# Kernel optimization log

Hardware: AMD Instinct MI355X
Metric: run time of the kernel (lower is better)

The kernel has to match this reference:

```python
import jax, jax.numpy as jnp
import numpy as np

MEAN = 0.1307
SIGMA = 0.3081
BINARY_ITER = 10
SIG_SCALE = 5.0


def spu(x):
    # SPU(x) = x^2 - 0.5 for x >= 0, sigmoid(-x) - 1 for x < 0 (continuous at 0)
    return jnp.where(x >= 0, x * x - 0.5, jax.nn.sigmoid(-x) - 1.0)


def joining_line(x1, y1, x2, y2):
    slope = (y2 - y1) / (x2 - x1)
    return slope, y2 - slope * x2


def parabola_tangent(x):
    return 2.0 * x, -x * x - 0.5


def parabola_tangent_through(x1, y1):
    D = 4.0 * x1 * x1 - 4.0 * y1 - 2.0
    x2 = (2.0 * x1 + jnp.sqrt(jnp.clip(D, 0.0))) / 2.0
    return parabola_tangent(x2)


def sigmoid_tangent(x):
    s = jax.nn.sigmoid(x)
    slope = -s * (1.0 - s)
    return slope, -s - slope * x


def binary_search_point(lx, ux, uy):
    L = lx
    R = jnp.zeros_like(lx)
    for _ in range(BINARY_ITER):  # fixed 10-iteration search, unrolled
        m = 0.5 * (L + R)
        sm, im = sigmoid_tangent(m)
        mask = sm * ux + im - uy > 0
        L = jnp.where(mask, m, L)
        R = jnp.where(mask, R, m)
    return L


def line_to_constraint(slope, intercept):
    # [n, n+1]: diagonal slope matrix with intercept as last column (matches torch diagflat/cat)
    return jnp.concatenate([jnp.diagflat(slope), intercept[:, None]], axis=1)


def analyze_affine(W, b, ub, lb):
    constr = jnp.concatenate([W, b[:, None]], axis=1)
    bu = jnp.where(W > 0, ub[None, :], lb[None, :])
    bl = jnp.where(W > 0, lb[None, :], ub[None, :])
    return constr, jnp.einsum('ij,ij->i', bu, W) + b, jnp.einsum('ij,ij->i', bl, W) + b


def analyze_spu(ux, lx):
    uy = spu(ux)
    ly = spu(lx)
    new_ub = jnp.maximum(uy, ly)
    sj, ij = joining_line(lx, ly, ux, uy)
    right = lx > 0
    left = ux <= 0
    crossing = (~left) & (~right)
    # learned positions at their (fresh) init: sigmoid(0) -> midpoint
    mid = 0.5 * (ux + lx)
    sp, ip = parabola_tangent(mid)
    ssm, ism = sigmoid_tangent(mid)
    new_lb = jnp.where(crossing, jnp.full_like(uy, -0.5), jnp.minimum(uy, ly))
    # crossing-case lower constraint
    spu_, ipu = parabola_tangent(ux)
    limit = spu_ * lx + ipu
    clm = (jnp.abs(lx) > ux).astype(lx.dtype)
    clp = jax.nn.sigmoid((clm - 0.5) * 2.0 * SIG_SCALE) * (ly - limit) + limit
    ptm = clp < -0.5
    spt, ipt = parabola_tangent_through(lx, clp)
    sjn, ijn = joining_line(lx, clp, jnp.zeros_like(lx), jnp.full_like(lx, -0.5))
    s_cl = jnp.where(ptm, spt, sjn)
    i_cl = jnp.where(ptm, ipt, ijn)
    # crossing-case upper constraint
    ssl, isl = sigmoid_tangent(lx)
    stv = ssl * ux + isl - uy
    L = binary_search_point(lx, ux, uy)
    scp = jax.nn.sigmoid(-SIG_SCALE) * (L - lx) + lx
    ssc, isc = sigmoid_tangent(scp)
    up_mask = stv > 0
    s_cu = jnp.where(up_mask, ssc, sj)
    i_cu = jnp.where(up_mask, isc, ij)
    rf = right.astype(lx.dtype)
    lf = left.astype(lx.dtype)
    cf = crossing.astype(lx.dtype)
    us = rf * sj + lf * ssm + cf * s_cu
    ui = rf * ij + lf * ism + cf * i_cu
    ls = rf * sp + lf * sj + cf * s_cl
    li = rf * ip + lf * ij + cf * i_cl
    return line_to_constraint(us, ui), line_to_constraint(ls, li), new_ub, new_lb


def back_substitute(uc, lc, ub, lb):
    cu, cl = uc[-1], lc[-1]
    for pu, pl in zip(uc[-2::-1], lc[-2::-1]):
        # where(curr>0, prev_upper, prev_lower) contracted with curr == split pos/neg matmuls
        Wu, bu = cu[:, :-1], cu[:, -1]
        cu = jnp.maximum(Wu, 0.0) @ pu + jnp.minimum(Wu, 0.0) @ pl
        cu = cu.at[:, -1].add(bu)
        Wl, bl = cl[:, :-1], cl[:, -1]
        cl = jnp.maximum(Wl, 0.0) @ pl + jnp.minimum(Wl, 0.0) @ pu
        cl = cl.at[:, -1].add(bl)
    return jnp.minimum(ub, cu[:, 0]), jnp.maximum(lb, cl[:, 0])


def setup_inputs() -> dict:
    key = jax.random.key(0)
    ks = jax.random.split(key, 9)
    d_in, h, d_out = 784, 2048, 10
    inputs = jax.random.uniform(ks[0], (d_in,), dtype=jnp.float32)
    eps = jnp.float32(0.05)
    w1 = jax.random.normal(ks[1], (h, d_in), dtype=jnp.float32) / np.sqrt(d_in).astype(np.float32)
    b1 = jax.random.normal(ks[2], (h,), dtype=jnp.float32) * 0.1
    w2 = jax.random.normal(ks[3], (h, h), dtype=jnp.float32) / np.sqrt(h).astype(np.float32)
    b2 = jax.random.normal(ks[4], (h,), dtype=jnp.float32) * 0.1
    w3 = jax.random.normal(ks[5], (h, h), dtype=jnp.float32) / np.sqrt(h).astype(np.float32)
    b3 = jax.random.normal(ks[6], (h,), dtype=jnp.float32) * 0.1
    w4 = jax.random.normal(ks[7], (d_out, h), dtype=jnp.float32) / np.sqrt(h).astype(np.float32)
    b4 = jax.random.normal(ks[8], (d_out,), dtype=jnp.float32) * 0.1
    return {"inputs": inputs, "eps": eps, "w1": w1, "b1": b1, "w2": w2, "b2": b2,
            "w3": w3, "b3": b3, "w4": w4, "b4": b4}


def reference(inputs, eps, w1, b1, w2, b2, w3, b3, w4, b4):
    ub = [jnp.clip(inputs + eps, None, 1.0)]
    lb = [jnp.clip(inputs - eps, 0.0)]
    # normalization layer: applied in place to bounds and input constraint ([784,1])
    uc = [((ub[0] - MEAN) / SIGMA)[:, None]]
    lc = [((lb[0] - MEAN) / SIGMA)[:, None]]
    ub[0] = (ub[0] - MEAN) / SIGMA
    lb[0] = (lb[0] - MEAN) / SIGMA
    weights = [(w1, b1), (w2, b2), (w3, b3), (w4, b4)]
    for i, (W, b) in enumerate(weights):
        c, u, l = analyze_affine(W, b, ub[-1], lb[-1])
        uc.append(c)
        lc.append(c)
        ub.append(u)
        lb.append(l)
        u, l = back_substitute(uc, lc, ub[-1], lb[-1])
        ub[-1], lb[-1] = u, l
        if i < len(weights) - 1:
            cu_, cl_, u, l = analyze_spu(ub[-1], lb[-1])
            uc.append(cu_)
            lc.append(cl_)
            ub.append(u)
            lb.append(l)
            u, l = back_substitute(uc, lc, ub[-1], lb[-1])
            ub[-1], lb[-1] = u, l
    return lb[-1].min()
```

## Files before the change

kernel.cpp:

```cpp
#include <hip/hip_runtime.h>
#include <cstdint>
#include <cstddef>

#define MEAN_C 0.1307f
#define SIGMA_C 0.3081f
#define SIG_SCALE_C 5.0f

typedef __bf16 bf16_t;
typedef __bf16 bf16x8 __attribute__((ext_vector_type(8)));
typedef __bf16 bf16x4 __attribute__((ext_vector_type(4)));
typedef float f32x4 __attribute__((ext_vector_type(4)));

__device__ __forceinline__ f32x4 mfma16(bf16x8 a, bf16x8 b, f32x4 c) {
    return __builtin_amdgcn_mfma_f32_16x16x32_bf16(a, b, c, 0, 0, 0);
}

typedef const __attribute__((address_space(1))) void* gvp;
typedef __attribute__((address_space(3))) void* lvp;
__device__ __forceinline__ void g2l16(const void* g, void* l) {
    __builtin_amdgcn_global_load_lds((gvp)g, (lvp)l, 16, 0, 0);
}

__device__ __forceinline__ size_t swz(int r, int k, int ktiles) {
    return (((size_t)(r >> 4) * ktiles + (k >> 5)) << 9)
         + (((k >> 3) & 3) << 7) + ((r & 15) << 3) + (k & 7);
}

#define KTILES 64


__device__ __forceinline__ float sigmoidf_(float x) {
    if (x >= 0.f) { float e = __expf(-x); return 1.f / (1.f + e); }
    float e = __expf(x); return e / (1.f + e);
}

__device__ __forceinline__ float spu_f(float x) {
    return (x >= 0.f) ? (x * x - 0.5f) : (sigmoidf_(-x) - 1.f);
}

__device__ __forceinline__ float wave_sum(float a) {
    #pragma unroll
    for (int o = 32; o > 0; o >>= 1) a += __shfl_xor(a, o, 64);
    return a;
}

__device__ __forceinline__ void spu_body(int i, int n,
        float iUi, float iLi, float vU, float vL,
        float* __restrict__ us, float* __restrict__ ui,
        float* __restrict__ ls, float* __restrict__ li,
        float* __restrict__ pU, float* __restrict__ pL) {
    float ux = fminf(iUi, vU);
    float lx = fmaxf(iLi, vL);
    float uy = spu_f(ux), ly = spu_f(lx);
    float new_ub = fmaxf(uy, ly);
    float sj = (uy - ly) / (ux - lx);
    float ij = uy - sj * ux;
    bool right = lx > 0.f;
    bool left = ux <= 0.f;
    float mid = 0.5f * (ux + lx);
    float sp = 2.f * mid, ip = -mid * mid - 0.5f;
    float sm = sigmoidf_(mid);
    float ssm = -sm * (1.f - sm);
    float ism = -sm - ssm * mid;
    bool crossing = (!left) && (!right);
    float new_lb = crossing ? -0.5f : fminf(uy, ly);
    float spu_s = 2.f * ux, ipu = -ux * ux - 0.5f;
    float limit = spu_s * lx + ipu;
    float clm = (fabsf(lx) > ux) ? 1.f : 0.f;
    float clp = sigmoidf_((clm - 0.5f) * 2.f * SIG_SCALE_C) * (ly - limit) + limit;
    bool ptm = clp < -0.5f;
    float D = 4.f * lx * lx - 4.f * clp - 2.f;
    float x2 = (2.f * lx + sqrtf(fmaxf(D, 0.f))) * 0.5f;
    float spt = 2.f * x2, ipt = -x2 * x2 - 0.5f;
    float sjn = (clp + 0.5f) / lx;
    float ijn = -0.5f;
    float s_cl = ptm ? spt : sjn;
    float i_cl = ptm ? ipt : ijn;
    float sl = sigmoidf_(lx);
    float ssl = -sl * (1.f - sl);
    float isl = -sl - ssl * lx;
    float stv = ssl * ux + isl - uy;
    float Lb = lx, Rb = 0.f;
    #pragma unroll
    for (int t = 0; t < 10; ++t) {
        float mm = 0.5f * (Lb + Rb);
        float smm = sigmoidf_(mm);
        float sms = -smm * (1.f - smm);
        float smi = -smm - sms * mm;
        bool mask = (sms * ux + smi - uy) > 0.f;
        Lb = mask ? mm : Lb;
        Rb = mask ? Rb : mm;
    }
    float scp = sigmoidf_(-SIG_SCALE_C) * (Lb - lx) + lx;
    float sc = sigmoidf_(scp);
    float ssc = -sc * (1.f - sc);
    float isc = -sc - ssc * scp;
    bool up = stv > 0.f;
    float s_cu = up ? ssc : sj;
    float i_cu = up ? isc : ij;
    float usv, uiv, lsv, liv;
    if (right)      { usv = sj;   uiv = ij;   lsv = sp;   liv = ip;   }
    else if (left)  { usv = ssm;  uiv = ism;  lsv = sj;   liv = ij;   }
    else            { usv = s_cu; uiv = i_cu; lsv = s_cl; liv = i_cl; }
    us[i] = usv; ui[i] = uiv; ls[i] = lsv; li[i] = liv;
    float vu = (usv >= 0.f) ? vU : vL;
    float vl = (lsv >= 0.f) ? vL : vU;
    pU[i] = fminf(new_ub, usv * vu + uiv);
    pL[i] = fmaxf(new_lb, lsv * vl + liv);
}


__global__ __launch_bounds__(256) void k_interval_affine(
        const float* __restrict__ W, const float* __restrict__ b,
        const float* __restrict__ U, const float* __restrict__ L,
        int m, int nrows, float* __restrict__ uo, float* __restrict__ lo) {
    int r = (blockIdx.x << 2) + (threadIdx.x >> 6);
    if (r >= nrows) return;
    int lane = threadIdx.x & 63;
    const f32x4* Wr = (const f32x4*)(W + (size_t)r * m);
    const f32x4* U4 = (const f32x4*)U;
    const f32x4* L4 = (const f32x4*)L;
    int nf4 = m >> 2;
    float au = 0.f, al = 0.f;
    for (int j = lane; j < nf4; j += 64) {
        f32x4 wv = Wr[j], uu = U4[j], ll = L4[j];
        #pragma unroll
        for (int u = 0; u < 4; ++u) {
            float w = wv[u];
            float hi = (w > 0.f) ? uu[u] : ll[u];
            float lo2 = (w > 0.f) ? ll[u] : uu[u];
            au = fmaf(w, hi, au);
            al = fmaf(w, lo2, al);
        }
    }
    au = wave_sum(au); al = wave_sum(al);
    if (lane == 0) { uo[r] = au + b[r]; lo[r] = al + b[r]; }
}

__global__ void k_spu2(const float* __restrict__ iU, const float* __restrict__ iL,
                       const float* __restrict__ vraw, int n,
                       float* __restrict__ us, float* __restrict__ ui,
                       float* __restrict__ ls, float* __restrict__ li,
                       float* __restrict__ pU, float* __restrict__ pL) {
    int i = blockIdx.x * blockDim.x + threadIdx.x;
    if (i >= n) return;
    spu_body(i, n, iU[i], iL[i], vraw[i], vraw[n + i], us, ui, ls, li, pU, pL);
}


__global__ __launch_bounds__(256) void k_wT3(
        const float* __restrict__ W1, const float* __restrict__ W2,
        const float* __restrict__ W3,
        bf16_t* __restrict__ W1t, bf16_t* __restrict__ W2t, bf16_t* __restrict__ W3t,
        const float* __restrict__ x, const float* __restrict__ eps,
        float* __restrict__ ubn, float* __restrict__ lbn) {
    __shared__ bf16_t t[64 * 65];
    int z = blockIdx.z;
    const float* W; int N, ldw; bf16_t* Wt;
    if (z == 0)      { W = W2; N = 2048; ldw = 2048; Wt = W2t; }
    else if (z == 1) { W = W3; N = 2048; ldw = 2048; Wt = W3t; }
    else {
        W = W1; N = 784; ldw = 784; Wt = W1t;
        if (blockIdx.y >= 14) {
            if (blockIdx.y == 14 && blockIdx.x == 0) {
                for (int i = threadIdx.x; i < 896; i += 256) {
                    if (i >= 784) { ubn[i] = 0.f; lbn[i] = 0.f; }
                    else {
                        float e = eps[0];
                        float ub = fminf(x[i] + e, 1.f);
                        float lb = fmaxf(x[i] - e, 0.f);
                        ubn[i] = (ub - MEAN_C) / SIGMA_C;
                        lbn[i] = (lb - MEAN_C) / SIGMA_C;
                    }
                }
            }
            return;
        }
    }
    int k0 = blockIdx.x * 64, n0 = blockIdx.y * 64;
    int tid = threadIdx.x;
    int rg = tid >> 4;
    int cg = (tid & 15) * 4;
    bool fast = (n0 + 64 <= N);
    #pragma unroll
    for (int it = 0; it < 4; ++it) {
        int row = it * 16 + rg;
        const float* Wr = W + (size_t)(k0 + row) * ldw + n0 + cg;
        float v0, v1, v2, v3;
        if (fast) {
            f32x4 vv = *(const f32x4*)Wr;
            v0 = vv[0]; v1 = vv[1]; v2 = vv[2]; v3 = vv[3];
        } else {
            v0 = (n0 + cg + 0 < N) ? Wr[0] : 0.f;
            v1 = (n0 + cg + 1 < N) ? Wr[1] : 0.f;
            v2 = (n0 + cg + 2 < N) ? Wr[2] : 0.f;
            v3 = (n0 + cg + 3 < N) ? Wr[3] : 0.f;
        }
        t[(cg + 0) * 65 + row] = (bf16_t)v0;
        t[(cg + 1) * 65 + row] = (bf16_t)v1;
        t[(cg + 2) * 65 + row] = (bf16_t)v2;
        t[(cg + 3) * 65 + row] = (bf16_t)v3;
    }
    __syncthreads();
    #pragma unroll
    for (int p = 0; p < 2; ++p) {
        int c = tid + p * 256;
        int lr = c & 63, lq = c >> 6;
        bf16x8 v;
        #pragma unroll
        for (int u = 0; u < 8; ++u) v[u] = t[lr * 65 + lq * 8 + u];
        *(bf16x8*)(Wt + swz(n0 + lr, k0 + lq * 8, KTILES)) = v;
    }
}

__global__ __launch_bounds__(256) void k_prep16(
        const float* __restrict__ W, const float* __restrict__ b, int n,
        const float* __restrict__ cus, const float* __restrict__ cui,
        const float* __restrict__ cls, const float* __restrict__ cli,
        const float* __restrict__ bvec,
        const float* __restrict__ U, const float* __restrict__ L,
        bf16_t* __restrict__ Ab, float* __restrict__ av,
        float* __restrict__ iU, float* __restrict__ iL) {
    int rt = blockIdx.x;
    int tid = threadIdx.x, lane = tid & 63, wid = tid >> 6;
    int mrow = lane & 15, q = lane >> 4;
    int r = rt * 16 + mrow;
    bool act = r < 2 * n;
    bool isU = r < n;
    int i = act ? (isU ? r : r - n) : 0;
    float gate = act ? 1.f : 0.f;
    const float* Wr = W + (size_t)i * 2048;
    const float* ps = isU ? cus : cls;
    const float* ns = isU ? cls : cus;
    const float* yi = isU ? cui : cli;
    const float* zi = isU ? cli : cui;
    const float* hi = isU ? U : L;
    const float* lo = isU ? L : U;
    float a = 0.f, a2 = 0.f;
    bf16_t* Abase = Ab + ((size_t)rt * KTILES) * 512 + lane * 8;
    for (int kt = wid; kt < KTILES; kt += 4) {
        int k0 = kt * 32 + q * 8;
        bf16x8 ov;
        #pragma unroll
        for (int h = 0; h < 2; ++h) {
            int kb = k0 + 4 * h;
            f32x4 wv = *(const f32x4*)(Wr + kb);
            f32x4 p0 = *(const f32x4*)(ps + kb);
            f32x4 q0 = *(const f32x4*)(ns + kb);
            f32x4 y0 = *(const f32x4*)(yi + kb);
            f32x4 z0 = *(const f32x4*)(zi + kb);
            f32x4 c0 = *(const f32x4*)(bvec + kb);
            f32x4 h0 = *(const f32x4*)(hi + kb);
            f32x4 l0 = *(const f32x4*)(lo + kb);
            #pragma unroll
            for (int u = 0; u < 4; ++u) {
                float w = gate * wv[u];
                float pos = fmaxf(w, 0.f), neg = fminf(w, 0.f);
                float mx = pos * p0[u] + neg * q0[u];
                ov[4 * h + u] = (bf16_t)mx;
                a += pos * y0[u] + neg * z0[u] + mx * c0[u];
                a2 += pos * h0[u] + neg * l0[u];
            }
        }
        *(bf16x8*)(Abase + (size_t)kt * 512) = ov;
    }
    a += __shfl_xor(a, 16, 64);  a += __shfl_xor(a, 32, 64);
    a2 += __shfl_xor(a2, 16, 64); a2 += __shfl_xor(a2, 32, 64);
    __shared__ float sh[2][4][16];
    if (lane < 16) { sh[0][wid][lane] = a; sh[1][wid][lane] = a2; }
    __syncthreads();
    if (tid < 16) {
        int r2 = rt * 16 + tid;
        float ta = sh[0][0][tid] + sh[0][1][tid] + sh[0][2][tid] + sh[0][3][tid];
        float tb = sh[1][0][tid] + sh[1][1][tid] + sh[1][2][tid] + sh[1][3][tid];
        if (r2 < 2 * n) {
            bool isU2 = r2 < n;
            int i2 = isU2 ? r2 : r2 - n;
            av[r2] = ta + b[i2];
            if (isU2) iU[i2] = tb + b[i2];
            else      iL[i2] = tb + b[i2];
        } else {
            av[r2] = 0.f;
        }
    }
}

__global__ __launch_bounds__(256) void k_colmix16(
        const bf16_t* __restrict__ Cb, int ldc, int splits, size_t sstride, int n,
        int tpb,
        const float* __restrict__ cus, const float* __restrict__ cui,
        const float* __restrict__ cls, const float* __restrict__ cli,
        const float* __restrict__ bvec,
        bf16_t* __restrict__ Ab, float* __restrict__ av) {
    int rt = blockIdx.x;
    int kt0 = blockIdx.y * tpb;
    int tid = threadIdx.x, lane = tid & 63, wid = tid >> 6;
    int mrow = lane & 15, q = lane >> 4;
    int r = rt * 16 + mrow;
    bool isU = r < n;
    const bf16_t* Cr = Cb + (size_t)r * ldc;
    const float* ps = isU ? cus : cls;
    const float* ns = isU ? cls : cus;
    const float* yi = isU ? cui : cli;
    const float* zi = isU ? cli : cui;
    float a = 0.f;
    bf16_t* Abase = Ab + ((size_t)rt * KTILES) * 512 + lane * 8;
    for (int kt = kt0 + wid; kt < kt0 + tpb; kt += 4) {
        int k0 = kt * 32 + q * 8;
        float wsum[8] = {0.f, 0.f, 0.f, 0.f, 0.f, 0.f, 0.f, 0.f};
        for (int s = 0; s < splits; ++s) {
            bf16x8 v = *(const bf16x8*)(Cr + s * sstride + k0);
            #pragma unroll
            for (int u = 0; u < 8; ++u) wsum[u] += (float)v[u];
        }
        f32x4 p0 = *(const f32x4*)(ps + k0), p1 = *(const f32x4*)(ps + k0 + 4);
        f32x4 q0 = *(const f32x4*)(ns + k0), q1 = *(const f32x4*)(ns + k0 + 4);
        f32x4 y0 = *(const f32x4*)(yi + k0), y1 = *(const f32x4*)(yi + k0 + 4);
        f32x4 z0 = *(const f32x4*)(zi + k0), z1 = *(const f32x4*)(zi + k0 + 4);
        f32x4 c0 = *(const f32x4*)(bvec + k0), c1 = *(const f32x4*)(bvec + k0 + 4);
        bf16x8 ov;
        #pragma unroll
        for (int u = 0; u < 4; ++u) {
            float w = wsum[u];
            float pos = fmaxf(w, 0.f), neg = fminf(w, 0.f);
            float mx = pos * p0[u] + neg * q0[u];
            ov[u] = (bf16_t)mx;
            a += pos * y0[u] + neg * z0[u] + mx * c0[u];
        }
        #pragma unroll
        for (int u = 0; u < 4; ++u) {
            float w = wsum[4 + u];
            float pos = fmaxf(w, 0.f), neg = fminf(w, 0.f);
            float mx = pos * p1[u] + neg * q1[u];
            ov[4 + u] = (bf16_t)mx;
            a += pos * y1[u] + neg * z1[u] + mx * c1[u];
        }
        *(bf16x8*)(Abase + (size_t)kt * 512) = ov;
    }
    a += __shfl_xor(a, 16, 64);
    a += __shfl_xor(a, 32, 64);
    __shared__ float sh[4][16];
    if (lane < 16) sh[wid][lane] = a;
    __syncthreads();
    if (tid < 16) {
        float tot = sh[0][tid] + sh[1][tid] + sh[2][tid] + sh[3][tid];
        atomicAdd(&av[rt * 16 + tid], tot);
    }
}

__global__ __launch_bounds__(640) void k_reduce16f(
        const bf16_t* __restrict__ Cb, int ldc, int m, int n,
        int splits, size_t sstride,
        const float* __restrict__ av,
        const float* __restrict__ ubn, const float* __restrict__ lbn,
        const float* __restrict__ iL,
        float* __restrict__ out) {
    __shared__ float sbl[16];
    int tid = threadIdx.x, lane = tid & 63, wv = tid >> 6;
    int nch = m >> 3;
    int i = wv;
    int r = n + i;
    const bf16_t* Cr = Cb + (size_t)r * ldc;
    const float* p = lbn;
    const float* q = ubn;
    float a = 0.f;
    for (int c = lane; c < nch; c += 64) {
        float wsum[8] = {0.f, 0.f, 0.f, 0.f, 0.f, 0.f, 0.f, 0.f};
        for (int s = 0; s < splits; ++s) {
            bf16x8 v = *(const bf16x8*)(Cr + s * sstride + c * 8);
            #pragma unroll
            for (int u = 0; u < 8; ++u) wsum[u] += (float)v[u];
        }
        f32x4 p0 = *(const f32x4*)(p + c * 8), p1 = *(const f32x4*)(p + c * 8 + 4);
        f32x4 q0 = *(const f32x4*)(q + c * 8), q1 = *(const f32x4*)(q + c * 8 + 4);
        #pragma unroll
        for (int u = 0; u < 4; ++u) {
            a += fmaxf(wsum[u], 0.f) * p0[u] + fminf(wsum[u], 0.f) * q0[u];
            a += fmaxf(wsum[4 + u], 0.f) * p1[u] + fminf(wsum[4 + u], 0.f) * q1[u];
        }
    }
    a = wave_sum(a);
    if (lane == 0) sbl[i] = fmaxf(iL[i], a + av[r]);
    __syncthreads();
    if (tid < 64) {
        float v = 3.4e38f;
        for (int j = lane; j < n; j += 64) v = fminf(v, sbl[j]);
        #pragma unroll
        for (int o = 32; o > 0; o >>= 1) v = fminf(v, __shfl_down(v, o, 64));
        if (lane == 0) out[0] = v;
    }
}


#define GEMM_PIPE()                                                            \
    int tid = threadIdx.x, lane = tid & 63, w = tid >> 6;                      \
    int wm = w & 1, wn = w >> 1;                                               \
    f32x4 acc[4][4];                                                           \
    _Pragma("unroll")                                                          \
    for (int i = 0; i < 4; ++i)                                                \
        _Pragma("unroll")                                                      \
        for (int j = 0; j < 4; ++j) acc[i][j] = (f32x4){0.f, 0.f, 0.f, 0.f};   \
    auto stage = [&](int kk) {                                                 \
        int b = kk & 1;                                                        \
        size_t go = (size_t)kk * 1024;                                         \
        bf16_t* la = &As2[b * 8192 + w * 1024];                                \
        bf16_t* lb = &Bs2[b * 8192 + w * 1024];                                \
        g2l16(a0 + go, la);          g2l16(a0 + go + 512, la + 512);           \
        g2l16(a1 + go, la + 4096);   g2l16(a1 + go + 512, la + 4608);          \
        g2l16(b0 + go, lb);          g2l16(b0 + go + 512, lb + 512);           \
        g2l16(b1 + go, lb + 4096);   g2l16(b1 + go + 512, lb + 4608);          \
    };                                                                         \
    stage(0); stage(1);                                                        \
    asm volatile("s_waitcnt vmcnt(8)" ::: "memory");                           \
    __builtin_amdgcn_s_barrier();                                              \
    for (int kk = 0; kk < nk; ++kk) {                                          \
        const bf16_t* cA = &As2[(kk & 1) * 8192];                              \
        const bf16_t* cB = &Bs2[(kk & 1) * 8192];                              \
        bf16x8 af0[4], af1[4], bq0[4], bq1[4];                                 \
        _Pragma("unroll")                                                      \
        for (int i = 0; i < 4; ++i) {                                          \
            af0[i] = *(const bf16x8*)(cA + (wm * 4 + i) * 1024 + lane * 8);    \
            af1[i] = *(const bf16x8*)(cA + (wm * 4 + i) * 1024 + 512 + lane * 8); \
            bq0[i] = *(const bf16x8*)(cB + (wn * 4 + i) * 1024 + lane * 8);    \
            bq1[i] = *(const bf16x8*)(cB + (wn * 4 + i) * 1024 + 512 + lane * 8); \
        }                                                                      \
        asm volatile("s_waitcnt lgkmcnt(0)" ::: "memory");                     \
        __builtin_amdgcn_s_barrier();                                          \
        if (kk + 2 < nk) stage(kk + 2);                                        \
        _Pragma("unroll")                                                      \
        for (int i = 0; i < 4; ++i)                                            \
            _Pragma("unroll")                                                  \
            for (int j = 0; j < 4; ++j)                                        \
                acc[i][j] = mfma16(bq0[j], af0[i], acc[i][j]);                 \
        _Pragma("unroll")                                                      \
        for (int i = 0; i < 4; ++i)                                            \
            _Pragma("unroll")                                                  \
            for (int j = 0; j < 4; ++j)                                        \
                acc[i][j] = mfma16(bq1[j], af1[i], acc[i][j]);                 \
        if (kk + 2 < nk) asm volatile("s_waitcnt vmcnt(8)" ::: "memory");      \
        else             asm volatile("s_waitcnt vmcnt(0)" ::: "memory");      \
        __builtin_amdgcn_s_barrier();                                          \
    }

__global__ __launch_bounds__(256) void k_gemm16(
        const bf16_t* __restrict__ A, const bf16_t* __restrict__ Bt,
        bf16_t* __restrict__ C, int ldc, size_t sstride, int nk) {
    __shared__ __align__(16) bf16_t As2[16384];
    __shared__ __align__(16) bf16_t Bs2[16384];
    int tr0 = blockIdx.y * 8, tc0 = blockIdx.x * 8;
    int kt0 = blockIdx.z * nk * 2;
    int wtmp = threadIdx.x >> 6, ltmp = threadIdx.x & 63;
    const bf16_t* a0 = A + (((size_t)(tr0 + wtmp)     * KTILES + kt0) << 9) + ltmp * 8;
    const bf16_t* a1 = A + (((size_t)(tr0 + wtmp + 4) * KTILES + kt0) << 9) + ltmp * 8;
    const bf16_t* b0 = Bt + (((size_t)(tc0 + wtmp)     * KTILES + kt0) << 9) + ltmp * 8;
    const bf16_t* b1 = Bt + (((size_t)(tc0 + wtmp + 4) * KTILES + kt0) << 9) + ltmp * 8;
    GEMM_PIPE()
    bf16_t* Cz = C + (size_t)blockIdx.z * sstride;
    int orow = lane & 15, ocol = (lane >> 4) * 4;
    size_t row0 = (size_t)blockIdx.y * 128;
    size_t col0 = (size_t)blockIdx.x * 128;
    #pragma unroll
    for (int i = 0; i < 4; ++i) {
        size_t gr = row0 + wm * 64 + i * 16 + orow;
        #pragma unroll
        for (int j = 0; j < 4; ++j) {
            size_t gc = col0 + wn * 64 + j * 16 + ocol;
            bf16x4 v;
            #pragma unroll
            for (int rg = 0; rg < 4; ++rg) v[rg] = (bf16_t)acc[i][j][rg];
            *(bf16x4*)(Cz + gr * (size_t)ldc + gc) = v;
        }
    }
}

__global__ __launch_bounds__(256) void k_gemm16_mix(
        const bf16_t* __restrict__ A, const bf16_t* __restrict__ Bt, int n,
        const float* __restrict__ cus, const float* __restrict__ cui,
        const float* __restrict__ cls, const float* __restrict__ cli,
        const float* __restrict__ bvec,
        bf16_t* __restrict__ Ab2, float* __restrict__ av, int nk) {
    __shared__ __align__(16) bf16_t As2[16384];
    __shared__ __align__(16) bf16_t Bs2[16384];
    __shared__ float asum[2][128];
    int wg = (int)(blockIdx.y * gridDim.x + blockIdx.x);
    int xcd = wg & 7, idx = wg >> 3;
    int bm = (xcd & 3) * 8 + (idx & 7);
    int bn = (xcd >> 2) * 8 + (idx >> 3);
    int tr0 = bm * 8, tc0 = bn * 8;
    int wtmp = threadIdx.x >> 6, ltmp = threadIdx.x & 63;
    const bf16_t* a0 = A + (((size_t)(tr0 + wtmp)     * KTILES) << 9) + ltmp * 8;
    const bf16_t* a1 = A + (((size_t)(tr0 + wtmp + 4) * KTILES) << 9) + ltmp * 8;
    const bf16_t* b0 = Bt + (((size_t)(tc0 + wtmp)     * KTILES) << 9) + ltmp * 8;
    const bf16_t* b1 = Bt + (((size_t)(tc0 + wtmp + 4) * KTILES) << 9) + ltmp * 8;
    GEMM_PIPE()
    size_t row0 = (size_t)bm * 128;
    size_t col0 = (size_t)bn * 128;
    bool isU = (int)row0 < n;
    const float* ps = isU ? cus : cls;
    const float* ns = isU ? cls : cus;
    const float* yi = isU ? cui : cli;
    const float* zi = isU ? cli : cui;
    int orow = lane & 15, ocol = (lane >> 4) * 4;
    #pragma unroll
    for (int i = 0; i < 4; ++i) {
        int gr = (int)row0 + wm * 64 + i * 16 + orow;
        float ra = 0.f;
        #pragma unroll
        for (int j = 0; j < 4; ++j) {
            int gc = (int)col0 + wn * 64 + j * 16 + ocol;
            f32x4 p0 = *(const f32x4*)(ps + gc);
            f32x4 q0 = *(const f32x4*)(ns + gc);
            f32x4 y0 = *(const f32x4*)(yi + gc);
            f32x4 z0 = *(const f32x4*)(zi + gc);
            f32x4 c0 = *(const f32x4*)(bvec + gc);
            bf16x4 ov;
            #pragma unroll
            for (int rg = 0; rg < 4; ++rg) {
                float v = acc[i][j][rg];
                float pos = fmaxf(v, 0.f), neg = fminf(v, 0.f);
                float mx = pos * p0[rg] + neg * q0[rg];
                ov[rg] = (bf16_t)mx;
                ra += pos * y0[rg] + neg * z0[rg] + mx * c0[rg];
            }
            *(bf16x4*)(Ab2 + swz(gr, gc, KTILES)) = ov;
        }
        ra += __shfl_xor(ra, 16, 64);
        ra += __shfl_xor(ra, 32, 64);
        if (lane < 16) asum[wn][wm * 64 + i * 16 + lane] = ra;
    }
    __syncthreads();
    if (tid < 128) atomicAdd(&av[row0 + tid], asum[0][tid] + asum[1][tid]);
}

__global__ __launch_bounds__(256) void k_gemm16_red(
        const bf16_t* __restrict__ A, const bf16_t* __restrict__ Bt, int n,
        const float* __restrict__ ubn, const float* __restrict__ lbn,
        float* __restrict__ av, int nk) {
    __shared__ __align__(16) bf16_t As2[16384];
    __shared__ __align__(16) bf16_t Bs2[16384];
    __shared__ float asum[2][128];
    int wg = (int)(blockIdx.y * gridDim.x + blockIdx.x);
    int id = (wg & 7) * 28 + (wg >> 3);
    int bm = id / 7, bn = id % 7;
    int tr0 = bm * 8, tc0 = bn * 8;
    int wtmp = threadIdx.x >> 6, ltmp = threadIdx.x & 63;
    const bf16_t* a0 = A + (((size_t)(tr0 + wtmp)     * KTILES) << 9) + ltmp * 8;
    const bf16_t* a1 = A + (((size_t)(tr0 + wtmp + 4) * KTILES) << 9) + ltmp * 8;
    const bf16_t* b0 = Bt + (((size_t)(tc0 + wtmp)     * KTILES) << 9) + ltmp * 8;
    const bf16_t* b1 = Bt + (((size_t)(tc0 + wtmp + 4) * KTILES) << 9) + ltmp * 8;
    GEMM_PIPE()
    size_t row0 = (size_t)bm * 128;
    size_t col0 = (size_t)bn * 128;
    bool isU = (int)row0 < n;
    const float* p = isU ? ubn : lbn;
    const float* q = isU ? lbn : ubn;
    int ocol = (lane >> 4) * 4;
    #pragma unroll
    for (int i = 0; i < 4; ++i) {
        float ra = 0.f;
        #pragma unroll
        for (int j = 0; j < 4; ++j) {
            int gc = (int)col0 + wn * 64 + j * 16 + ocol;
            f32x4 p0 = *(const f32x4*)(p + gc);
            f32x4 q0 = *(const f32x4*)(q + gc);
            #pragma unroll
            for (int rg = 0; rg < 4; ++rg) {
                float v = acc[i][j][rg];
                ra += fmaxf(v, 0.f) * p0[rg] + fminf(v, 0.f) * q0[rg];
            }
        }
        ra += __shfl_xor(ra, 16, 64);
        ra += __shfl_xor(ra, 32, 64);
        if (lane < 16) asum[wn][wm * 64 + i * 16 + lane] = ra;
    }
    __syncthreads();
    if (tid < 128) atomicAdd(&av[row0 + tid], asum[0][tid] + asum[1][tid]);
}


extern "C" void kernel_launch(void* const* d_in, const int* in_sizes, int n_in,
                              void* d_out, int out_size, void* d_ws, size_t ws_size,
                              hipStream_t stream) {
    (void)in_sizes; (void)n_in; (void)out_size; (void)ws_size;
    const float* x   = (const float*)d_in[0];
    const float* eps = (const float*)d_in[1];
    const float* W1  = (const float*)d_in[2];
    const float* B1  = (const float*)d_in[3];
    const float* W2  = (const float*)d_in[4];
    const float* B2  = (const float*)d_in[5];
    const float* W3  = (const float*)d_in[6];
    const float* B3  = (const float*)d_in[7];
    const float* W4  = (const float*)d_in[8];
    const float* B4  = (const float*)d_in[9];
    float* out = (float*)d_out;

    const int H = 2048, DIN = 784, DOUT = 10;
    const int NP1 = 896;
    const int MP4 = 128;

    float* ws = (float*)d_ws;
    size_t off = 0;
    auto alloc = [&](size_t nf) -> float* {
        float* p = ws + off;
        off += (nf + 3) & ~(size_t)3;
        return p;
    };
    float* ubn = alloc(NP1);
    float* lbn = alloc(NP1);
    float* vraw1 = alloc(2 * H);
    float* us1 = alloc(H); float* ui1 = alloc(H); float* ls1 = alloc(H); float* li1 = alloc(H);
    float* pU1 = alloc(H); float* pL1 = alloc(H);
    float* iU2 = alloc(H); float* iL2 = alloc(H);
    float* us2 = alloc(H); float* ui2 = alloc(H); float* ls2 = alloc(H); float* li2 = alloc(H);
    float* pU2 = alloc(H); float* pL2 = alloc(H);
    float* iU3 = alloc(H); float* iL3 = alloc(H);
    float* us3 = alloc(H); float* ui3 = alloc(H); float* ls3 = alloc(H); float* li3 = alloc(H);
    float* pU3 = alloc(H); float* pL3 = alloc(H);
    float* iU4 = alloc(32); float* iL4 = alloc(32);
    float* av  = alloc(2 * H);
    bf16_t* Ab  = (bf16_t*)alloc((size_t)2 * H * H / 2);
    bf16_t* Ab2 = (bf16_t*)alloc((size_t)2 * H * H / 2);
    bf16_t* W1t = (bf16_t*)alloc((size_t)NP1 * H / 2);
    bf16_t* W2t = (bf16_t*)alloc((size_t)H * H / 2);
    bf16_t* W3t = (bf16_t*)alloc((size_t)H * H / 2);
    bf16_t* Cs  = (bf16_t*)alloc((size_t)16 * MP4 * H / 2);

    dim3 blk(256);

    k_wT3<<<dim3(32, 32, 3), blk, 0, stream>>>(W1, W2, W3, W1t, W2t, W3t,
                                               x, eps, ubn, lbn);

    size_t ss4H = (size_t)MP4 * H;
    size_t ss4N = (size_t)MP4 * NP1;

    k_interval_affine<<<dim3(H / 4), blk, 0, stream>>>(W1, B1, ubn, lbn, DIN, H,
                                                       vraw1, vraw1 + H);
    k_spu2<<<dim3(H / 64), dim3(64), 0, stream>>>(vraw1, vraw1 + H, vraw1, H,
        us1, ui1, ls1, li1, pU1, pL1);

    k_prep16<<<dim3(2 * H / 16), blk, 0, stream>>>(W2, B2, H,
        us1, ui1, ls1, li1, B1, pU1, pL1, Ab, av, iU2, iL2);
    k_gemm16_red<<<dim3(2 * H / 128, NP1 / 128), blk, 0, stream>>>(Ab, W1t, H,
        ubn, lbn, av, KTILES / 2);
    k_spu2<<<dim3(H / 64), dim3(64), 0, stream>>>(iU2, iL2, av, H,
        us2, ui2, ls2, li2, pU2, pL2);

    k_prep16<<<dim3(2 * H / 16), blk, 0, stream>>>(W3, B3, H,
        us2, ui2, ls2, li2, B2, pU2, pL2, Ab, av, iU3, iL3);
    k_gemm16_mix<<<dim3(2 * H / 128, H / 128), blk, 0, stream>>>(Ab, W2t, H,
        us1, ui1, ls1, li1, B1, Ab2, av, KTILES / 2);
    k_gemm16_red<<<dim3(2 * H / 128, NP1 / 128), blk, 0, stream>>>(Ab2, W1t, H,
        ubn, lbn, av, KTILES / 2);
    k_spu2<<<dim3(H / 64), dim3(64), 0, stream>>>(iU3, iL3, av, H,
        us3, ui3, ls3, li3, pU3, pL3);

    k_prep16<<<dim3(MP4 / 16), blk, 0, stream>>>(W4, B4, DOUT,
        us3, ui3, ls3, li3, B3, pU3, pL3, Ab, av, iU4, iL4);
    k_gemm16<<<dim3(H / 128, MP4 / 128, 16), blk, 0, stream>>>(Ab, W3t, Cs, H, ss4H, 2);
    k_colmix16<<<dim3(MP4 / 16, 8), blk, 0, stream>>>(Cs, H, 16, ss4H, DOUT, KTILES / 8,
        us2, ui2, ls2, li2, B2, Ab2, av);
    k_gemm16<<<dim3(H / 128, MP4 / 128, 16), blk, 0, stream>>>(Ab2, W2t, Cs, H, ss4H, 2);
    k_colmix16<<<dim3(MP4 / 16, 8), blk, 0, stream>>>(Cs, H, 16, ss4H, DOUT, KTILES / 8,
        us1, ui1, ls1, li1, B1, Ab, av);
    k_gemm16<<<dim3(NP1 / 128, MP4 / 128, 16), blk, 0, stream>>>(Ab, W1t, Cs, NP1, ss4N, 2);
    k_reduce16f<<<dim3(1), dim3(640), 0, stream>>>(Cs, NP1, DIN, DOUT, 16, ss4N,
        av, ubn, lbn, iL4, out);
}
```

Before: 329.5 us.

## Use 8-wave blocks in fused GEMMs and fuse first affine with SPU

The fused back-substitution GEMMs (mix and red) now launch 512 threads (8 waves) per 128x128 tile instead of 4. Each wave owns a 64x32 sub-tile and loads half as many LDS stages, which lowers per-wave accumulator registers and adds latency hiding. The epilogue reductions are widened to four column groups to match. Separately, the first interval-affine kernel now applies the SPU relaxation directly, removing one launch and an intermediate buffer.

```diff
diff --git a/kernel.cpp b/kernel.cpp
--- a/kernel.cpp
+++ b/kernel.cpp
@@ -110,12 +110,15 @@
 }
 
 
-__global__ __launch_bounds__(256) void k_interval_affine(
+__global__ __launch_bounds__(256) void k_interval_spu(
         const float* __restrict__ W, const float* __restrict__ b,
         const float* __restrict__ U, const float* __restrict__ L,
-        int m, int nrows, float* __restrict__ uo, float* __restrict__ lo) {
+        int m, int n,
+        float* __restrict__ us, float* __restrict__ ui,
+        float* __restrict__ ls, float* __restrict__ li,
+        float* __restrict__ pU, float* __restrict__ pL) {
     int r = (blockIdx.x << 2) + (threadIdx.x >> 6);
-    if (r >= nrows) return;
+    if (r >= n) return;
     int lane = threadIdx.x & 63;
     const f32x4* Wr = (const f32x4*)(W + (size_t)r * m);
     const f32x4* U4 = (const f32x4*)U;
@@ -134,7 +137,10 @@
         }
     }
     au = wave_sum(au); al = wave_sum(al);
-    if (lane == 0) { uo[r] = au + b[r]; lo[r] = al + b[r]; }
+    if (lane == 0) {
+        float vU = au + b[r], vL = al + b[r];
+        spu_body(r, n, vU, vL, vU, vL, us, ui, ls, li, pU, pL);
+    }
 }
 
 __global__ void k_spu2(const float* __restrict__ iU, const float* __restrict__ iL,
@@ -391,7 +397,6 @@
     }
 }
 
-
 #define GEMM_PIPE()                                                            \
     int tid = threadIdx.x, lane = tid & 63, w = tid >> 6;                      \
     int wm = w & 1, wn = w >> 1;                                               \
@@ -473,7 +478,58 @@
     }
 }
 
-__global__ __launch_bounds__(256) void k_gemm16_mix(
+#define GEMM_PIPE8()                                                           \
+    int tid = threadIdx.x, lane = tid & 63, w = tid >> 6;            \
+    int wm = w >> 2, wn = w & 3;                                               \
+    f32x4 acc[4][2];                                                           \
+    _Pragma("unroll")                                                          \
+    for (int i = 0; i < 4; ++i)                                                \
+        _Pragma("unroll")                                                      \
+        for (int j = 0; j < 2; ++j) acc[i][j] = (f32x4){0.f, 0.f, 0.f, 0.f};   \
+    auto stage = [&](int kk) {                                                 \
+        int b = kk & 1;                                                        \
+        size_t go = (size_t)kk * 1024;                                         \
+        bf16_t* la = &As2[b * 8192 + w * 1024];                                \
+        bf16_t* lb = &Bs2[b * 8192 + w * 1024];                                \
+        g2l16(a0 + go, la);   g2l16(a0 + go + 512, la + 512);                  \
+        g2l16(b0 + go, lb);   g2l16(b0 + go + 512, lb + 512);                  \
+    };                                                                         \
+    stage(0); stage(1);                                                        \
+    asm volatile("s_waitcnt vmcnt(4)" ::: "memory");                           \
+    __builtin_amdgcn_s_barrier();                                              \
+    for (int kk = 0; kk < nk; ++kk) {                                          \
+        const bf16_t* cA = &As2[(kk & 1) * 8192];                              \
+        const bf16_t* cB = &Bs2[(kk & 1) * 8192];                              \
+        bf16x8 af0[4], af1[4], bq0[2], bq1[2];                                 \
+        _Pragma("unroll")                                                      \
+        for (int i = 0; i < 4; ++i) {                                          \
+            af0[i] = *(const bf16x8*)(cA + (wm * 4 + i) * 1024 + lane * 8);    \
+            af1[i] = *(const bf16x8*)(cA + (wm * 4 + i) * 1024 + 512 + lane * 8); \
+        }                                                                      \
+        _Pragma("unroll")                                                      \
+        for (int j = 0; j < 2; ++j) {                                          \
+            bq0[j] = *(const bf16x8*)(cB + (wn * 2 + j) * 1024 + lane * 8);    \
+            bq1[j] = *(const bf16x8*)(cB + (wn * 2 + j) * 1024 + 512 + lane * 8); \
+        }                                                                      \
+        asm volatile("s_waitcnt lgkmcnt(0)" ::: "memory");                     \
+        __builtin_amdgcn_s_barrier();                                          \
+        if (kk + 2 < nk) stage(kk + 2);                                        \
+        _Pragma("unroll")                                                      \
+        for (int i = 0; i < 4; ++i)                                            \
+            _Pragma("unroll")                                                  \
+            for (int j = 0; j < 2; ++j)                                        \
+                acc[i][j] = mfma16(bq0[j], af0[i], acc[i][j]);                 \
+        _Pragma("unroll")                                                      \
+        for (int i = 0; i < 4; ++i)                                            \
+            _Pragma("unroll")                                                  \
+            for (int j = 0; j < 2; ++j)                                        \
+                acc[i][j] = mfma16(bq1[j], af1[i], acc[i][j]);                 \
+        if (kk + 2 < nk) asm volatile("s_waitcnt vmcnt(4)" ::: "memory");      \
+        else             asm volatile("s_waitcnt vmcnt(0)" ::: "memory");      \
+        __builtin_amdgcn_s_barrier();                                          \
+    }
+
+__global__ __launch_bounds__(512, 4) void k_gemm16_mix(
         const bf16_t* __restrict__ A, const bf16_t* __restrict__ Bt, int n,
         const float* __restrict__ cus, const float* __restrict__ cui,
         const float* __restrict__ cls, const float* __restrict__ cli,
@@ -481,18 +537,16 @@
         bf16_t* __restrict__ Ab2, float* __restrict__ av, int nk) {
     __shared__ __align__(16) bf16_t As2[16384];
     __shared__ __align__(16) bf16_t Bs2[16384];
-    __shared__ float asum[2][128];
+    __shared__ float asum[4][128];
     int wg = (int)(blockIdx.y * gridDim.x + blockIdx.x);
     int xcd = wg & 7, idx = wg >> 3;
     int bm = (xcd & 3) * 8 + (idx & 7);
     int bn = (xcd >> 2) * 8 + (idx >> 3);
     int tr0 = bm * 8, tc0 = bn * 8;
     int wtmp = threadIdx.x >> 6, ltmp = threadIdx.x & 63;
-    const bf16_t* a0 = A + (((size_t)(tr0 + wtmp)     * KTILES) << 9) + ltmp * 8;
-    const bf16_t* a1 = A + (((size_t)(tr0 + wtmp + 4) * KTILES) << 9) + ltmp * 8;
-    const bf16_t* b0 = Bt + (((size_t)(tc0 + wtmp)     * KTILES) << 9) + ltmp * 8;
-    const bf16_t* b1 = Bt + (((size_t)(tc0 + wtmp + 4) * KTILES) << 9) + ltmp * 8;
-    GEMM_PIPE()
+    const bf16_t* a0 = A + (((size_t)(tr0 + wtmp) * KTILES) << 9) + ltmp * 8;
+    const bf16_t* b0 = Bt + (((size_t)(tc0 + wtmp) * KTILES) << 9) + ltmp * 8;
+    GEMM_PIPE8()
     size_t row0 = (size_t)bm * 128;
     size_t col0 = (size_t)bn * 128;
     bool isU = (int)row0 < n;
@@ -506,8 +560,8 @@
         int gr = (int)row0 + wm * 64 + i * 16 + orow;
         float ra = 0.f;
         #pragma unroll
-        for (int j = 0; j < 4; ++j) {
-            int gc = (int)col0 + wn * 64 + j * 16 + ocol;
+        for (int j = 0; j < 2; ++j) {
+            int gc = (int)col0 + wn * 32 + j * 16 + ocol;
             f32x4 p0 = *(const f32x4*)(ps + gc);
             f32x4 q0 = *(const f32x4*)(ns + gc);
             f32x4 y0 = *(const f32x4*)(yi + gc);
@@ -529,26 +583,26 @@
         if (lane < 16) asum[wn][wm * 64 + i * 16 + lane] = ra;
     }
     __syncthreads();
-    if (tid < 128) atomicAdd(&av[row0 + tid], asum[0][tid] + asum[1][tid]);
-}
-
-__global__ __launch_bounds__(256) void k_gemm16_red(
+    if (tid < 128)
+        atomicAdd(&av[row0 + tid],
+                  asum[0][tid] + asum[1][tid] + asum[2][tid] + asum[3][tid]);
+}
+
+__global__ __launch_bounds__(512, 4) void k_gemm16_red(
         const bf16_t* __restrict__ A, const bf16_t* __restrict__ Bt, int n,
         const float* __restrict__ ubn, const float* __restrict__ lbn,
         float* __restrict__ av, int nk) {
     __shared__ __align__(16) bf16_t As2[16384];
     __shared__ __align__(16) bf16_t Bs2[16384];
-    __shared__ float asum[2][128];
+    __shared__ float asum[4][128];
     int wg = (int)(blockIdx.y * gridDim.x + blockIdx.x);
     int id = (wg & 7) * 28 + (wg >> 3);
     int bm = id / 7, bn = id % 7;
     int tr0 = bm * 8, tc0 = bn * 8;
     int wtmp = threadIdx.x >> 6, ltmp = threadIdx.x & 63;
-    const bf16_t* a0 = A + (((size_t)(tr0 + wtmp)     * KTILES) << 9) + ltmp * 8;
-    const bf16_t* a1 = A + (((size_t)(tr0 + wtmp + 4) * KTILES) << 9) + ltmp * 8;
-    const bf16_t* b0 = Bt + (((size_t)(tc0 + wtmp)     * KTILES) << 9) + ltmp * 8;
-    const bf16_t* b1 = Bt + (((size_t)(tc0 + wtmp + 4) * KTILES) << 9) + ltmp * 8;
-    GEMM_PIPE()
+    const bf16_t* a0 = A + (((size_t)(tr0 + wtmp) * KTILES) << 9) + ltmp * 8;
+    const bf16_t* b0 = Bt + (((size_t)(tc0 + wtmp) * KTILES) << 9) + ltmp * 8;
+    GEMM_PIPE8()
     size_t row0 = (size_t)bm * 128;
     size_t col0 = (size_t)bn * 128;
     bool isU = (int)row0 < n;
@@ -559,8 +613,8 @@
     for (int i = 0; i < 4; ++i) {
         float ra = 0.f;
         #pragma unroll
-        for (int j = 0; j < 4; ++j) {
-            int gc = (int)col0 + wn * 64 + j * 16 + ocol;
+        for (int j = 0; j < 2; ++j) {
+            int gc = (int)col0 + wn * 32 + j * 16 + ocol;
             f32x4 p0 = *(const f32x4*)(p + gc);
             f32x4 q0 = *(const f32x4*)(q + gc);
             #pragma unroll
@@ -574,7 +628,9 @@
         if (lane < 16) asum[wn][wm * 64 + i * 16 + lane] = ra;
     }
     __syncthreads();
-    if (tid < 128) atomicAdd(&av[row0 + tid], asum[0][tid] + asum[1][tid]);
+    if (tid < 128)
+        atomicAdd(&av[row0 + tid],
+                  asum[0][tid] + asum[1][tid] + asum[2][tid] + asum[3][tid]);
 }
 
 
@@ -607,7 +663,6 @@
     };
     float* ubn = alloc(NP1);
     float* lbn = alloc(NP1);
-    float* vraw1 = alloc(2 * H);
     float* us1 = alloc(H); float* ui1 = alloc(H); float* ls1 = alloc(H); float* li1 = alloc(H);
     float* pU1 = alloc(H); float* pL1 = alloc(H);
     float* iU2 = alloc(H); float* iL2 = alloc(H);
@@ -633,23 +688,21 @@
     size_t ss4H = (size_t)MP4 * H;
     size_t ss4N = (size_t)MP4 * NP1;
 
-    k_interval_affine<<<dim3(H / 4), blk, 0, stream>>>(W1, B1, ubn, lbn, DIN, H,
-                                                       vraw1, vraw1 + H);
-    k_spu2<<<dim3(H / 64), dim3(64), 0, stream>>>(vraw1, vraw1 + H, vraw1, H,
+    k_interval_spu<<<dim3(H / 4), blk, 0, stream>>>(W1, B1, ubn, lbn, DIN, H,
         us1, ui1, ls1, li1, pU1, pL1);
 
     k_prep16<<<dim3(2 * H / 16), blk, 0, stream>>>(W2, B2, H,
         us1, ui1, ls1, li1, B1, pU1, pL1, Ab, av, iU2, iL2);
-    k_gemm16_red<<<dim3(2 * H / 128, NP1 / 128), blk, 0, stream>>>(Ab, W1t, H,
+    k_gemm16_red<<<dim3(2 * H / 128, NP1 / 128), dim3(512), 0, stream>>>(Ab, W1t, H,
         ubn, lbn, av, KTILES / 2);
     k_spu2<<<dim3(H / 64), dim3(64), 0, stream>>>(iU2, iL2, av, H,
         us2, ui2, ls2, li2, pU2, pL2);
 
     k_prep16<<<dim3(2 * H / 16), blk, 0, stream>>>(W3, B3, H,
         us2, ui2, ls2, li2, B2, pU2, pL2, Ab, av, iU3, iL3);
-    k_gemm16_mix<<<dim3(2 * H / 128, H / 128), blk, 0, stream>>>(Ab, W2t, H,
+    k_gemm16_mix<<<dim3(2 * H / 128, H / 128), dim3(512), 0, stream>>>(Ab, W2t, H,
         us1, ui1, ls1, li1, B1, Ab2, av, KTILES / 2);
-    k_gemm16_red<<<dim3(2 * H / 128, NP1 / 128), blk, 0, stream>>>(Ab2, W1t, H,
+    k_gemm16_red<<<dim3(2 * H / 128, NP1 / 128), dim3(512), 0, stream>>>(Ab2, W1t, H,
         ubn, lbn, av, KTILES / 2);
     k_spu2<<<dim3(H / 64), dim3(64), 0, stream>>>(iU3, iL3, av, H,
         us3, ui3, ls3, li3, pU3, pL3);
```

Result: no change. 330.7 us (+0.3%).
